# Performance work log

Measured on AMD Instinct MI355X. Metric: run time of the kernel, lower is better.

The kernel has to match this reference:

```python
import jax, jax.numpy as jnp
import numpy as np

N_NODES = 50000
N_EDGES = 800000
NODE_IN = 16
NODE_OUT = 3
H = 128
N_LAYERS = 3


def setup_inputs() -> dict:
    key = jax.random.key(0)
    ks = jax.random.split(key, 16)
    s = 0.05
    inp = {
        "x": jax.random.normal(ks[0], (N_NODES, NODE_IN), dtype=jnp.float32),
        "edge_index": jax.random.randint(ks[1], (2, N_EDGES), 0, N_NODES, dtype=jnp.int64),
        # encoder / decoder
        "enc_w": jax.random.normal(ks[2], (NODE_IN, H), dtype=jnp.float32) * s,
        "enc_b": jnp.zeros((H,), dtype=jnp.float32),
        "dec_w": jax.random.normal(ks[3], (H, NODE_OUT), dtype=jnp.float32) * s,
        "dec_b": jnp.zeros((NODE_OUT,), dtype=jnp.float32),
        # 3 processor layers, edge MLP: Linear(2H,H) -> ReLU -> Linear(H,H)
        "edge_w1": jax.random.normal(ks[4], (N_LAYERS, 2 * H, H), dtype=jnp.float32) * s,
        "edge_b1": jnp.zeros((N_LAYERS, H), dtype=jnp.float32),
        "edge_w2": jax.random.normal(ks[5], (N_LAYERS, H, H), dtype=jnp.float32) * s,
        "edge_b2": jnp.zeros((N_LAYERS, H), dtype=jnp.float32),
        # node MLP: Linear(2H,H) -> ReLU -> Linear(H,H)
        "node_w1": jax.random.normal(ks[6], (N_LAYERS, 2 * H, H), dtype=jnp.float32) * s,
        "node_b1": jnp.zeros((N_LAYERS, H), dtype=jnp.float32),
        "node_w2": jax.random.normal(ks[7], (N_LAYERS, H, H), dtype=jnp.float32) * s,
        "node_b2": jnp.zeros((N_LAYERS, H), dtype=jnp.float32),
    }
    return inp


def reference(x, edge_index, enc_w, enc_b, dec_w, dec_b,
              edge_w1, edge_b1, edge_w2, edge_b2,
              node_w1, node_b1, node_w2, node_b2):
    row = edge_index[0]  # source nodes
    col = edge_index[1]  # destination nodes
    h = x @ enc_w + enc_b  # [N, H]
    for l in range(N_LAYERS):
        # EdgeModel: cat(src, dest) -> MLP
        e_in = jnp.concatenate([h[row], h[col]], axis=1)  # [E, 2H]
        e = jnp.maximum(e_in @ edge_w1[l] + edge_b1[l], 0.0) @ edge_w2[l] + edge_b2[l]  # [E, H]
        # NodeModel: scatter_add messages by col, cat with x -> MLP
        agg = jax.ops.segment_sum(e, col, num_segments=h.shape[0])  # [N, H]
        n_in = jnp.concatenate([h, agg], axis=1)  # [N, 2H]
        h_upd = jnp.maximum(n_in @ node_w1[l] + node_b1[l], 0.0) @ node_w2[l] + node_b2[l]
        h = h + h_upd  # residual
    return h @ dec_w + dec_b  # [N, NODE_OUT]
```

## Files before the change

### kernel.cpp

```cpp
#include <hip/hip_runtime.h>
#include <hip/hip_bf16.h>
#include <stdint.h>

#define N_NODES 50000
#define N_EDGES 800000
#define HID 128
#define NODE_IN 16
#define NODE_OUT 3
#define NODE_TILES 782
#define SCAN_BLOCKS 196
#define EDGE_BLOCKS 3125
#define MFOLD_BLOCKS 192
#define DGB 16
#define EDBLOCKS 3125

typedef __attribute__((ext_vector_type(8))) short short8;
typedef __attribute__((ext_vector_type(4))) float f32x4;
typedef __attribute__((ext_vector_type(4))) unsigned int u32x4;

__device__ __forceinline__ unsigned short f2bf(float f) {
    union { float f; unsigned int u; } v; v.f = f;
    unsigned int u = v.u;
    u += 0x7fff + ((u >> 16) & 1);
    return (unsigned short)(u >> 16);
}
__device__ __forceinline__ float bf2f(unsigned short s) {
    union { unsigned int u; float f; } v; v.u = ((unsigned int)s) << 16;
    return v.f;
}
__device__ __forceinline__ float bfu_lo(unsigned int u) {
    union { unsigned int u; float f; } v; v.u = u << 16; return v.f;
}
__device__ __forceinline__ float bfu_hi(unsigned int u) {
    union { unsigned int u; float f; } v; v.u = u & 0xffff0000u; return v.f;
}
__device__ __forceinline__ unsigned int cvt_pk_bf16(float lo, float hi) {
    unsigned int r;
    asm("v_cvt_pk_bf16_f32 %0, %1, %2" : "=v"(r) : "v"(lo), "v"(hi));
    return r;
}

__global__ __launch_bounds__(256) void k1_fused(
    const int* __restrict__ colp, int* __restrict__ cnt, int* __restrict__ rank,
    const float* __restrict__ edge_w2, const float* __restrict__ node_w1,
    const float* __restrict__ edge_b2,
    float* __restrict__ Mtmp, float* __restrict__ Vtmp,
    const float* __restrict__ x, const float* __restrict__ enc_w,
    const float* __restrict__ enc_b, unsigned short* __restrict__ h) {
    __shared__ float wts[NODE_IN * HID];
    __shared__ float bts[HID];
    __shared__ float xs[64][NODE_IN];
    int b = blockIdx.x, t = threadIdx.x;
    if (b < EDGE_BLOCKS) {
        int e = b * 256 + t;
        rank[e] = atomicAdd(&cnt[colp[e]], 1);
    } else if (b < EDGE_BLOCKS + MFOLD_BLOCKS) {
        int d = (b - EDGE_BLOCKS) * 256 + t;
        int L = d / 16384, rem = d & 16383;
        int k = rem >> 7, n = rem & 127;
        const float* w2  = edge_w2 + (size_t)L * 16384;
        const float* w1b = node_w1 + (size_t)L * 32768 + 16384;
        float acc = 0.f;
        #pragma unroll 4
        for (int j = 0; j < 128; j++) acc += w2[k * 128 + j] * w1b[j * 128 + n];
        Mtmp[d] = acc;
        if (k == 0) {
            const float* b2 = edge_b2 + (size_t)L * 128;
            float vv = 0.f;
            #pragma unroll 4
            for (int j = 0; j < 128; j++) vv += b2[j] * w1b[j * 128 + n];
            Vtmp[L * 128 + n] = vv;
        }
    } else {
        int b2 = b - EDGE_BLOCKS - MFOLD_BLOCKS;
        int n0 = b2 * 64;
        for (int i = t; i < NODE_IN * HID; i += 256) wts[i] = enc_w[i];
        if (t < HID) bts[t] = enc_b[t];
        for (int i = t; i < 64 * NODE_IN; i += 256) {
            int nl = i >> 4, ii = i & 15;
            int n = n0 + nl;
            xs[nl][ii] = (n < N_NODES) ? x[n * NODE_IN + ii] : 0.f;
        }
        __syncthreads();
        for (int o = t; o < 64 * HID; o += 256) {
            int nl = o >> 7, cc = o & 127;
            float acc = bts[cc];
            #pragma unroll
            for (int i = 0; i < NODE_IN; i++) acc += xs[nl][i] * wts[i * HID + cc];
            int n = n0 + nl;
            if (n < N_NODES) h[n * HID + cc] = f2bf(acc);
        }
    }
}

__global__ __launch_bounds__(256) void k2a_scan1_swizzle(
    const int* __restrict__ cnt, int* __restrict__ ex, int* __restrict__ bsums,
    const float* __restrict__ edge_w1, const float* __restrict__ node_w1,
    const float* __restrict__ node_w2, const float* __restrict__ Mtmp,
    unsigned short* __restrict__ swz) {
    __shared__ int s[256];
    int b = blockIdx.x, t = threadIdx.x;
    if (b < SCAN_BLOCKS) {
        int i = b * 256 + t;
        int v = (i < N_NODES) ? cnt[i] : 0;
        s[t] = v;
        __syncthreads();
        for (int off = 1; off < 256; off <<= 1) {
            int u = (t >= off) ? s[t - off] : 0;
            __syncthreads();
            s[t] += u;
            __syncthreads();
        }
        if (i < N_NODES) ex[i] = s[t] - v;
        if (t == 255) bsums[b] = s[255];
    } else {
        for (int d = (b - SCAN_BLOCKS) * 256 + t; d < 3 * 98304;
             d += (gridDim.x - SCAN_BLOCKS) * 256) {
            int L = d / 98304;
            int rem = d - L * 98304;
            unsigned short* base = swz + L * 98304;
            if (rem < 32768) {
                const float* w1 = edge_w1 + (size_t)L * 32768;
                int j = rem & 7, ll = (rem >> 3) & 63, tt = rem >> 9;
                int nt = tt & 15, kt = tt >> 4;
                int k = kt * 32 + ((ll >> 4) << 3) + j;
                int cc = nt * 16 + (ll & 15);
                float v = (cc < 128) ? w1[k * 128 + cc] : w1[(128 + k) * 128 + (cc - 128)];
                base[rem] = f2bf(v);
            } else if (rem < 49152) {
            } else if (rem < 81920) {
                int d2 = rem - 49152;
                int j = d2 & 7, ll = (d2 >> 3) & 63, tt = d2 >> 9;
                int nt = tt & 7, kt = tt >> 3;
                int k = kt * 32 + ((ll >> 4) << 3) + j, n = (nt << 4) + (ll & 15);
                float v = (k < 128) ? node_w1[(size_t)L * 32768 + k * 128 + n]
                                    : Mtmp[(size_t)L * 16384 + (k - 128) * 128 + n];
                base[rem] = f2bf(v);
            } else {
                int d2 = rem - 81920;
                const float* src = node_w2 + (size_t)L * 16384;
                int j = d2 & 7, ll = (d2 >> 3) & 63, tt = d2 >> 9;
                int nt = tt & 7, kt = tt >> 3;
                int k = kt * 32 + ((ll >> 4) << 3) + j, n = (nt << 4) + (ll & 15);
                base[rem] = f2bf(src[k * 128 + n]);
            }
        }
    }
}

__global__ __launch_bounds__(256) void k3_scatter_sd(
    const int* __restrict__ rowp, const int* __restrict__ colp,
    const int* __restrict__ ex, const int* __restrict__ bsums,
    const int* __restrict__ rank, int* __restrict__ rsrt, int* __restrict__ ex2,
    const unsigned short* __restrict__ h, const unsigned short* __restrict__ w1c,
    const float* __restrict__ eb1,
    unsigned short* __restrict__ S, unsigned short* __restrict__ D) {
    __shared__ int sc[256];
    __shared__ int ls[SCAN_BLOCKS];
    __shared__ unsigned short hs[64][136];
    int b = blockIdx.x, t = threadIdx.x;
    if (b < EDGE_BLOCKS) {
        int v = (t < SCAN_BLOCKS) ? bsums[t] : 0;
        sc[t] = v;
        __syncthreads();
        for (int off = 1; off < 256; off <<= 1) {
            int u = (t >= off) ? sc[t - off] : 0;
            __syncthreads();
            sc[t] += u;
            __syncthreads();
        }
        if (t < SCAN_BLOCKS) ls[t] = sc[t] - v;
        __syncthreads();

        if (b < SCAN_BLOCKS) {
            int i = b * 256 + t;
            if (i < N_NODES) ex2[i] = ex[i] + ls[b];
        }
        int e = b * 256 + t;
        int c = colp[e];
        int pos = ex[c] + ls[c >> 8] + rank[e];
        rsrt[pos] = rowp[e];
    } else {
        int b2 = b - EDGE_BLOCKS;
        int wave = t >> 6, l = t & 63, q = l >> 4, l16 = l & 15;
        int nt0s = wave * 4;
        int n0 = b2 * 64;
        for (int i = t; i < 64 * 16; i += 256) {
            int nl = i >> 4, li = i & 15;
            int n = n0 + nl;
            short8 v = (short8){0, 0, 0, 0, 0, 0, 0, 0};
            if (n < N_NODES) v = *(const short8*)(h + (size_t)n * HID + li * 8);
            *(short8*)&hs[nl][li * 8] = v;
        }
        short8 wr[4][4];
        #pragma unroll
        for (int kt = 0; kt < 4; kt++)
            #pragma unroll
            for (int i = 0; i < 4; i++)
                wr[kt][i] = *(const short8*)(w1c + ((kt * 16 + nt0s + i) * 64 + l) * 8);
        __syncthreads();

        f32x4 acc[4][4];
        #pragma unroll
        for (int g = 0; g < 4; g++)
            #pragma unroll
            for (int i = 0; i < 4; i++) acc[g][i] = (f32x4){0.f, 0.f, 0.f, 0.f};
        #pragma unroll
        for (int kt = 0; kt < 4; kt++) {
            #pragma unroll
            for (int g = 0; g < 4; g++) {
                short8 a = *(const short8*)&hs[g * 16 + l16][kt * 32 + q * 8];
                #pragma unroll
                for (int i = 0; i < 4; i++)
                    acc[g][i] = __builtin_amdgcn_mfma_f32_16x16x32_bf16(a, wr[kt][i], acc[g][i], 0, 0, 0);
            }
        }
        #pragma unroll
        for (int i = 0; i < 4; i++) {
            int cc = (nt0s + i) * 16 + l16;
            float badd = 0.f;
            if (cc >= 128) badd = eb1[cc - 128];
            #pragma unroll
            for (int g = 0; g < 4; g++)
                #pragma unroll
                for (int r = 0; r < 4; r++) {
                    int n = n0 + g * 16 + q * 4 + r;
                    if (n < N_NODES) {
                        unsigned short v = f2bf(acc[g][i][r] + badd);
                        if (cc < 128) S[n * HID + cc] = v;
                        else          D[n * HID + (cc - 128)] = v;
                    }
                }
        }
    }
}

__global__ __launch_bounds__(256, 8) void edge_kernel(
    const unsigned short* __restrict__ S, const unsigned short* __restrict__ D,
    const int* __restrict__ rsrt, const int* __restrict__ ex2,
    float* __restrict__ aggH)
{
    int t = threadIdx.x;
    int g16 = t >> 4, ch = t & 15;

    const int q = EDBLOCKS / 8, r = EDBLOCKS % 8;
    int xcd = blockIdx.x & 7, slot = blockIdx.x >> 3;
    int cntx = q + (xcd < r);
    if (slot >= cntx) return;
    int myb = xcd * q + (xcd < r ? xcd : r) + slot;

    int d = myb * DGB + g16;
    int e0 = ex2[d];
    int e1 = (d < N_NODES - 1) ? ex2[d + 1] : N_EDGES;

    short8 dv = *(const short8*)(D + (size_t)d * HID + ch * 8);
    float dr[8];
    #pragma unroll
    for (int p = 0; p < 4; p++) {
        unsigned int ud = ((const unsigned int*)&dv)[p];
        dr[2 * p]     = bfu_lo(ud);
        dr[2 * p + 1] = bfu_hi(ud);
    }

    float a[8];
    #pragma unroll
    for (int j = 0; j < 8; j++) a[j] = 0.f;

    auto ldS = [&](int e) -> short8 {
        int rn = rsrt[e];
        return *(const short8*)(S + (size_t)rn * HID + ch * 8);
    };
    auto accum = [&](const short8& sv) {
        #pragma unroll
        for (int p = 0; p < 4; p++) {
            unsigned int us = ((const unsigned int*)&sv)[p];
            float v0 = bfu_lo(us) + dr[2 * p];
            float v1 = bfu_hi(us) + dr[2 * p + 1];
            v0 = v0 > 0.f ? v0 : 0.f;
            v1 = v1 > 0.f ? v1 : 0.f;
            a[2 * p]     += v0;
            a[2 * p + 1] += v1;
        }
    };

    int e = e0;
    short8 s0 = (short8){0, 0, 0, 0, 0, 0, 0, 0};
    short8 s1 = s0;
    if (e < e1)     s0 = ldS(e);
    if (e + 1 < e1) s1 = ldS(e + 1);
    for (; e + 2 < e1; e += 2) {
        short8 n0v = ldS(e + 2);
        short8 n1v = (e + 3 < e1) ? ldS(e + 3) : (short8){0, 0, 0, 0, 0, 0, 0, 0};
        accum(s0);
        accum(s1);
        s0 = n0v;
        s1 = n1v;
    }
    if (e < e1)     accum(s0);
    if (e + 1 < e1) accum(s1);

    f32x4* dst = (f32x4*)(aggH + (size_t)d * HID + ch * 8);
    dst[0] = (f32x4){a[0], a[1], a[2], a[3]};
    dst[1] = (f32x4){a[4], a[5], a[6], a[7]};
}

template<int LAST>
__global__ __launch_bounds__(256, 4) void node_kernel(
    unsigned short* __restrict__ h, float* __restrict__ aggH, const int* __restrict__ cnt,
    const unsigned short* __restrict__ w1m_s, const float* __restrict__ b1,
    const float* __restrict__ vfold,
    const unsigned short* __restrict__ w2s, const float* __restrict__ b2,
    const unsigned short* __restrict__ w1c_next, const float* __restrict__ eb1n,
    unsigned short* __restrict__ S, unsigned short* __restrict__ D,
    const float* __restrict__ dec_w, const float* __restrict__ dec_b, float* __restrict__ out)
{
    __shared__ unsigned short in_h[64][136];
    __shared__ unsigned short in_a[64][136];
    __shared__ int cnt_s[64];
    __shared__ float dw[HID * NODE_OUT];
    __shared__ float db[NODE_OUT];
    int t = threadIdx.x, wave = t >> 6, l = t & 63, q = l >> 4, l16 = l & 15;
    int nt0 = wave * 2, nt0s = wave * 4;
    int n0 = blockIdx.x * 64;

    if (LAST) {
        for (int i = t; i < HID * NODE_OUT; i += 256) dw[i] = dec_w[i];
        if (t < NODE_OUT) db[t] = dec_b[t];
    }

    #pragma unroll
    for (int it = 0; it < 8; it++) {
        int g = it * 256 + t;
        int nl = g >> 5, sub = g & 31, half = sub >> 4, li = sub & 15;
        int n = n0 + nl;
        short8 v = (short8){0, 0, 0, 0, 0, 0, 0, 0};
        if (n < N_NODES) {
            if (half == 0) {
                v = *(const short8*)(h + n * HID + li * 8);
            } else {
                const float* ap = aggH + n * HID + li * 8;
                f32x4 a0 = *(const f32x4*)ap, a1 = *(const f32x4*)(ap + 4);
                unsigned int* vp = (unsigned int*)&v;
                vp[0] = cvt_pk_bf16(a0[0], a0[1]);
                vp[1] = cvt_pk_bf16(a0[2], a0[3]);
                vp[2] = cvt_pk_bf16(a1[0], a1[1]);
                vp[3] = cvt_pk_bf16(a1[2], a1[3]);
            }
        }
        if (half == 0) *(short8*)&in_h[nl][li * 8] = v;
        else           *(short8*)&in_a[nl][li * 8] = v;
    }
    if (t < 64) cnt_s[t] = (n0 + t < N_NODES) ? cnt[n0 + t] : 0;
    __syncthreads();

    float b1r0 = b1[nt0 * 16 + l16], b1r1 = b1[(nt0 + 1) * 16 + l16];
    float vr0 = vfold[nt0 * 16 + l16], vr1 = vfold[(nt0 + 1) * 16 + l16];
    float b2r0 = b2[nt0 * 16 + l16], b2r1 = b2[(nt0 + 1) * 16 + l16];

    f32x4 acc[4][2];
    #pragma unroll
    for (int g = 0; g < 4; g++)
        #pragma unroll
        for (int j = 0; j < 2; j++) acc[g][j] = (f32x4){0.f, 0.f, 0.f, 0.f};
    #pragma unroll
    for (int kt = 0; kt < 8; kt++) {
        short8 b0 = *(const short8*)(w1m_s + ((kt * 8 + nt0)     * 64 + l) * 8);
        short8 b1v = *(const short8*)(w1m_s + ((kt * 8 + nt0 + 1) * 64 + l) * 8);
        #pragma unroll
        for (int g = 0; g < 4; g++) {
            short8 a = (kt < 4) ? *(const short8*)&in_h[g * 16 + l16][kt * 32 + q * 8]
                                : *(const short8*)&in_a[g * 16 + l16][(kt - 4) * 32 + q * 8];
            acc[g][0] = __builtin_amdgcn_mfma_f32_16x16x32_bf16(a, b0, acc[g][0], 0, 0, 0);
            acc[g][1] = __builtin_amdgcn_mfma_f32_16x16x32_bf16(a, b1v, acc[g][1], 0, 0, 0);
        }
    }
    __syncthreads();

    #pragma unroll
    for (int j = 0; j < 2; j++) {
        float bv = j ? b1r1 : b1r0;
        float vv = j ? vr1 : vr0;
        #pragma unroll
        for (int g = 0; g < 4; g++)
            #pragma unroll
            for (int r = 0; r < 4; r++) {
                int m2 = g * 16 + q * 4 + r;
                float v = acc[g][j][r] + bv + (float)cnt_s[m2] * vv;
                v = v > 0.f ? v : 0.f;
                in_a[m2][(nt0 + j) * 16 + l16] = f2bf(v);
            }
    }
    __syncthreads();

    f32x4 acc2[4][2];
    #pragma unroll
    for (int g = 0; g < 4; g++)
        #pragma unroll
        for (int j = 0; j < 2; j++) acc2[g][j] = (f32x4){0.f, 0.f, 0.f, 0.f};
    #pragma unroll
    for (int kt = 0; kt < 4; kt++) {
        short8 b0 = *(const short8*)(w2s + ((kt * 8 + nt0)     * 64 + l) * 8);
        short8 b1v = *(const short8*)(w2s + ((kt * 8 + nt0 + 1) * 64 + l) * 8);
        #pragma unroll
        for (int g = 0; g < 4; g++) {
            short8 a = *(const short8*)&in_a[g * 16 + l16][kt * 32 + q * 8];
            acc2[g][0] = __builtin_amdgcn_mfma_f32_16x16x32_bf16(a, b0, acc2[g][0], 0, 0, 0);
            acc2[g][1] = __builtin_amdgcn_mfma_f32_16x16x32_bf16(a, b1v, acc2[g][1], 0, 0, 0);
        }
    }
    #pragma unroll
    for (int j = 0; j < 2; j++) {
        float bv = j ? b2r1 : b2r0;
        #pragma unroll
        for (int g = 0; g < 4; g++)
            #pragma unroll
            for (int r = 0; r < 4; r++) {
                float v = acc2[g][j][r] + bv;
                int m2 = g * 16 + q * 4 + r;
                int n = n0 + m2;
                if (n < N_NODES) {
                    int c = (nt0 + j) * 16 + l16;
                    unsigned short nh = f2bf(bf2f(in_h[m2][c]) + v);
                    if (!LAST) h[n * HID + c] = nh;
                    in_h[m2][c] = nh;
                }
            }
    }
    __syncthreads();

    if (!LAST) {
        #pragma unroll
        for (int p = 0; p < 2; p++) {
            short8 wr[4][2];
            #pragma unroll
            for (int kt = 0; kt < 4; kt++) {
                wr[kt][0] = *(const short8*)(w1c_next + ((kt * 16 + nt0s + p * 2)     * 64 + l) * 8);
                wr[kt][1] = *(const short8*)(w1c_next + ((kt * 16 + nt0s + p * 2 + 1) * 64 + l) * 8);
            }
            f32x4 accs[4][2];
            #pragma unroll
            for (int g = 0; g < 4; g++)
                #pragma unroll
                for (int i = 0; i < 2; i++) accs[g][i] = (f32x4){0.f, 0.f, 0.f, 0.f};
            #pragma unroll
            for (int kt = 0; kt < 4; kt++) {
                #pragma unroll
                for (int g = 0; g < 4; g++) {
                    short8 a = *(const short8*)&in_h[g * 16 + l16][kt * 32 + q * 8];
                    accs[g][0] = __builtin_amdgcn_mfma_f32_16x16x32_bf16(a, wr[kt][0], accs[g][0], 0, 0, 0);
                    accs[g][1] = __builtin_amdgcn_mfma_f32_16x16x32_bf16(a, wr[kt][1], accs[g][1], 0, 0, 0);
                }
            }
            #pragma unroll
            for (int i = 0; i < 2; i++) {
                int c = (nt0s + p * 2 + i) * 16 + l16;
                float badd = 0.f;
                if (c >= 128) badd = eb1n[c - 128];
                #pragma unroll
                for (int g = 0; g < 4; g++)
                    #pragma unroll
                    for (int r = 0; r < 4; r++) {
                        int n = n0 + g * 16 + q * 4 + r;
                        if (n < N_NODES) {
                            unsigned short v = f2bf(accs[g][i][r] + badd);
                            if (c < 128) S[n * HID + c] = v;
                            else         D[n * HID + (c - 128)] = v;
                        }
                    }
            }
        }
    } else {
        if (t < 64 * NODE_OUT) {
            int nl = t / 3, o = t - 3 * nl;
            int n = n0 + nl;
            if (n < N_NODES) {
                float a = db[o];
                #pragma unroll 4
                for (int k = 0; k < HID; k++) a += bf2f(in_h[nl][k]) * dw[k * 3 + o];
                out[n * 3 + o] = a;
            }
        }
    }
}

extern "C" void kernel_launch(void* const* d_in, const int* in_sizes, int n_in,
                              void* d_out, int out_size, void* d_ws, size_t ws_size,
                              hipStream_t stream) {
    const float* x       = (const float*)d_in[0];
    const int*   ei      = (const int*)d_in[1];
    const float* enc_w   = (const float*)d_in[2];
    const float* enc_b   = (const float*)d_in[3];
    const float* dec_w   = (const float*)d_in[4];
    const float* dec_b   = (const float*)d_in[5];
    const float* edge_w1 = (const float*)d_in[6];
    const float* edge_b1 = (const float*)d_in[7];
    const float* edge_w2 = (const float*)d_in[8];
    const float* edge_b2 = (const float*)d_in[9];
    const float* node_w1 = (const float*)d_in[10];
    const float* node_b1 = (const float*)d_in[11];
    const float* node_w2 = (const float*)d_in[12];
    const float* node_b2 = (const float*)d_in[13];

    char* ws = (char*)d_ws;
    unsigned short* h    = (unsigned short*)ws;
    float*          aggH = (float*)(ws + 12800000);
    unsigned short* swz  = (unsigned short*)(ws + 38400000);
    int* cnt             = (int*)(ws + 38989824);
    int* ex              = (int*)(ws + 39189824);
    int* bsums           = (int*)(ws + 39389824);
    int* rsrt            = (int*)(ws + 39390848);
    unsigned short* Sbuf = (unsigned short*)(ws + 45790848);
    unsigned short* Dbuf = (unsigned short*)(ws + 58590848);
    float* Mtmp          = (float*)(ws + 71390848);
    float* Vtmp          = (float*)(ws + 71587456);
    int* ex2             = (int*)(ws + 71588992);
    int* rank            = (int*)(ws + 72000000);

    const int* rowp = ei;
    const int* colp = ei + N_EDGES;

    hipMemsetAsync(cnt, 0, (size_t)N_NODES * 4, stream);

    k1_fused<<<EDGE_BLOCKS + MFOLD_BLOCKS + NODE_TILES, 256, 0, stream>>>(
        colp, cnt, rank, edge_w2, node_w1, edge_b2, Mtmp, Vtmp,
        x, enc_w, enc_b, h);
    k2a_scan1_swizzle<<<SCAN_BLOCKS + 288, 256, 0, stream>>>(cnt, ex, bsums, edge_w1,
                                                             node_w1, node_w2, Mtmp, swz);
    k3_scatter_sd<<<EDGE_BLOCKS + NODE_TILES, 256, 0, stream>>>(
        rowp, colp, ex, bsums, rank, rsrt, ex2,
        h, swz , edge_b1 , Sbuf, Dbuf);

    for (int L = 0; L < 3; L++) {
        unsigned short* base = swz + (size_t)L * 98304;
        unsigned short* next = swz + (size_t)(L + 1) * 98304;
        edge_kernel<<<3128, 256, 0, stream>>>(Sbuf, Dbuf, rsrt, ex2, aggH);
        if (L < 2) {
            node_kernel<0><<<NODE_TILES, 256, 0, stream>>>(
                h, aggH, cnt,
                base + 49152, node_b1 + (size_t)L * HID, Vtmp + (size_t)L * HID,
                base + 81920, node_b2 + (size_t)L * HID,
                next, edge_b1 + (size_t)(L + 1) * HID, Sbuf, Dbuf, dec_w, dec_b, (float*)d_out);
        } else {
            node_kernel<1><<<NODE_TILES, 256, 0, stream>>>(
                h, aggH, cnt,
                base + 49152, node_b1 + (size_t)L * HID, Vtmp + (size_t)L * HID,
                base + 81920, node_b2 + (size_t)L * HID,
                base , edge_b1 , Sbuf, Dbuf, dec_w, dec_b, (float*)d_out);
        }
    }
}
```

Measured before the change: 364.9 us.

## Store aggregates as bf16, deepen edge gather prefetch, split weight swizzle across kernels

The edge kernel now writes per-node aggregated messages as packed bf16 instead of fp32, halving the aggregate buffer traffic, and the node kernel reads them directly without converting. The edge gather loop is restructured with an 8-deep prefetch of source indices and 4-deep prefetch of S rows to hide gather latency. The edge_w1 and node_w2 swizzles move into the first fused kernel, leaving only the Mtmp-dependent node_w1 swizzle in the scan kernel. The bf16 aggregate adds rounding before the node MLP, and the extra prefetch raises register pressure.

Result: slower. 415.1 us (+13.7%).

```diff
diff --git a/kernel.cpp b/kernel.cpp
--- a/kernel.cpp
+++ b/kernel.cpp
@@ -11,6 +11,8 @@
 #define SCAN_BLOCKS 196
 #define EDGE_BLOCKS 3125
 #define MFOLD_BLOCKS 192
+#define SWZA_BLOCKS 576
+#define SWZB_BLOCKS 384
 #define DGB 16
 #define EDBLOCKS 3125
 
@@ -46,7 +48,9 @@
     const float* __restrict__ edge_b2,
     float* __restrict__ Mtmp, float* __restrict__ Vtmp,
     const float* __restrict__ x, const float* __restrict__ enc_w,
-    const float* __restrict__ enc_b, unsigned short* __restrict__ h) {
+    const float* __restrict__ enc_b, unsigned short* __restrict__ h,
+    const float* __restrict__ edge_w1, const float* __restrict__ node_w2,
+    unsigned short* __restrict__ swz) {
     __shared__ float wts[NODE_IN * HID];
     __shared__ float bts[HID];
     __shared__ float xs[64][NODE_IN];
@@ -71,7 +75,7 @@
             for (int j = 0; j < 128; j++) vv += b2[j] * w1b[j * 128 + n];
             Vtmp[L * 128 + n] = vv;
         }
-    } else {
+    } else if (b < EDGE_BLOCKS + MFOLD_BLOCKS + NODE_TILES) {
         int b2 = b - EDGE_BLOCKS - MFOLD_BLOCKS;
         int n0 = b2 * 64;
         for (int i = t; i < NODE_IN * HID; i += 256) wts[i] = enc_w[i];
@@ -90,13 +94,32 @@
             int n = n0 + nl;
             if (n < N_NODES) h[n * HID + cc] = f2bf(acc);
         }
+    } else {
+        int d = (b - EDGE_BLOCKS - MFOLD_BLOCKS - NODE_TILES) * 256 + t;
+        int L = d / 49152, rem2 = d - L * 49152;
+        unsigned short* base = swz + L * 98304;
+        if (rem2 < 32768) {
+            const float* w1 = edge_w1 + (size_t)L * 32768;
+            int j = rem2 & 7, ll = (rem2 >> 3) & 63, tt = rem2 >> 9;
+            int nt = tt & 15, kt = tt >> 4;
+            int k = kt * 32 + ((ll >> 4) << 3) + j;
+            int cc = nt * 16 + (ll & 15);
+            float v = (cc < 128) ? w1[k * 128 + cc] : w1[(128 + k) * 128 + (cc - 128)];
+            base[rem2] = f2bf(v);
+        } else {
+            int d2 = rem2 - 32768;
+            const float* src = node_w2 + (size_t)L * 16384;
+            int j = d2 & 7, ll = (d2 >> 3) & 63, tt = d2 >> 9;
+            int nt = tt & 7, kt = tt >> 3;
+            int k = kt * 32 + ((ll >> 4) << 3) + j, n = (nt << 4) + (ll & 15);
+            base[81920 + d2] = f2bf(src[k * 128 + n]);
+        }
     }
 }
 
 __global__ __launch_bounds__(256) void k2a_scan1_swizzle(
     const int* __restrict__ cnt, int* __restrict__ ex, int* __restrict__ bsums,
-    const float* __restrict__ edge_w1, const float* __restrict__ node_w1,
-    const float* __restrict__ node_w2, const float* __restrict__ Mtmp,
+    const float* __restrict__ node_w1, const float* __restrict__ Mtmp,
     unsigned short* __restrict__ swz) {
     __shared__ int s[256];
     int b = blockIdx.x, t = threadIdx.x;
@@ -114,37 +137,15 @@
         if (i < N_NODES) ex[i] = s[t] - v;
         if (t == 255) bsums[b] = s[255];
     } else {
-        for (int d = (b - SCAN_BLOCKS) * 256 + t; d < 3 * 98304;
-             d += (gridDim.x - SCAN_BLOCKS) * 256) {
-            int L = d / 98304;
-            int rem = d - L * 98304;
-            unsigned short* base = swz + L * 98304;
-            if (rem < 32768) {
-                const float* w1 = edge_w1 + (size_t)L * 32768;
-                int j = rem & 7, ll = (rem >> 3) & 63, tt = rem >> 9;
-                int nt = tt & 15, kt = tt >> 4;
-                int k = kt * 32 + ((ll >> 4) << 3) + j;
-                int cc = nt * 16 + (ll & 15);
-                float v = (cc < 128) ? w1[k * 128 + cc] : w1[(128 + k) * 128 + (cc - 128)];
-                base[rem] = f2bf(v);
-            } else if (rem < 49152) {
-            } else if (rem < 81920) {
-                int d2 = rem - 49152;
-                int j = d2 & 7, ll = (d2 >> 3) & 63, tt = d2 >> 9;
-                int nt = tt & 7, kt = tt >> 3;
-                int k = kt * 32 + ((ll >> 4) << 3) + j, n = (nt << 4) + (ll & 15);
-                float v = (k < 128) ? node_w1[(size_t)L * 32768 + k * 128 + n]
-                                    : Mtmp[(size_t)L * 16384 + (k - 128) * 128 + n];
-                base[rem] = f2bf(v);
-            } else {
-                int d2 = rem - 81920;
-                const float* src = node_w2 + (size_t)L * 16384;
-                int j = d2 & 7, ll = (d2 >> 3) & 63, tt = d2 >> 9;
-                int nt = tt & 7, kt = tt >> 3;
-                int k = kt * 32 + ((ll >> 4) << 3) + j, n = (nt << 4) + (ll & 15);
-                base[rem] = f2bf(src[k * 128 + n]);
-            }
-        }
+        int d = (b - SCAN_BLOCKS) * 256 + t;
+        int L = d / 32768, d2 = d - L * 32768;
+        unsigned short* base = swz + L * 98304;
+        int j = d2 & 7, ll = (d2 >> 3) & 63, tt = d2 >> 9;
+        int nt = tt & 7, kt = tt >> 3;
+        int k = kt * 32 + ((ll >> 4) << 3) + j, n = (nt << 4) + (ll & 15);
+        float v = (k < 128) ? node_w1[(size_t)L * 32768 + k * 128 + n]
+                            : Mtmp[(size_t)L * 16384 + (k - 128) * 128 + n];
+        base[49152 + d2] = f2bf(v);
     }
 }
 
@@ -238,7 +239,7 @@
 __global__ __launch_bounds__(256, 8) void edge_kernel(
     const unsigned short* __restrict__ S, const unsigned short* __restrict__ D,
     const int* __restrict__ rsrt, const int* __restrict__ ex2,
-    float* __restrict__ aggH)
+    unsigned short* __restrict__ aggB)
 {
     int t = threadIdx.x;
     int g16 = t >> 4, ch = t & 15;
@@ -254,6 +255,25 @@
     int e1 = (d < N_NODES - 1) ? ex2[d + 1] : N_EDGES;
 
     short8 dv = *(const short8*)(D + (size_t)d * HID + ch * 8);
+
+    auto Srow = [&](int rn) -> short8 {
+        return *(const short8*)(S + (size_t)rn * HID + ch * 8);
+    };
+    const short8 z = (short8){0, 0, 0, 0, 0, 0, 0, 0};
+
+    int ra0 = (e0     < e1) ? rsrt[e0]     : 0;
+    int ra1 = (e0 + 1 < e1) ? rsrt[e0 + 1] : 0;
+    int ra2 = (e0 + 2 < e1) ? rsrt[e0 + 2] : 0;
+    int ra3 = (e0 + 3 < e1) ? rsrt[e0 + 3] : 0;
+    int rb0 = (e0 + 4 < e1) ? rsrt[e0 + 4] : 0;
+    int rb1 = (e0 + 5 < e1) ? rsrt[e0 + 5] : 0;
+    int rb2 = (e0 + 6 < e1) ? rsrt[e0 + 6] : 0;
+    int rb3 = (e0 + 7 < e1) ? rsrt[e0 + 7] : 0;
+    short8 c0 = (e0     < e1) ? Srow(ra0) : z;
+    short8 c1 = (e0 + 1 < e1) ? Srow(ra1) : z;
+    short8 c2 = (e0 + 2 < e1) ? Srow(ra2) : z;
+    short8 c3 = (e0 + 3 < e1) ? Srow(ra3) : z;
+
     float dr[8];
     #pragma unroll
     for (int p = 0; p < 4; p++) {
@@ -261,52 +281,54 @@
         dr[2 * p]     = bfu_lo(ud);
         dr[2 * p + 1] = bfu_hi(ud);
     }
-
     float a[8];
     #pragma unroll
     for (int j = 0; j < 8; j++) a[j] = 0.f;
 
-    auto ldS = [&](int e) -> short8 {
-        int rn = rsrt[e];
-        return *(const short8*)(S + (size_t)rn * HID + ch * 8);
-    };
     auto accum = [&](const short8& sv) {
         #pragma unroll
         for (int p = 0; p < 4; p++) {
             unsigned int us = ((const unsigned int*)&sv)[p];
             float v0 = bfu_lo(us) + dr[2 * p];
             float v1 = bfu_hi(us) + dr[2 * p + 1];
-            v0 = v0 > 0.f ? v0 : 0.f;
-            v1 = v1 > 0.f ? v1 : 0.f;
-            a[2 * p]     += v0;
-            a[2 * p + 1] += v1;
+            a[2 * p]     += v0 > 0.f ? v0 : 0.f;
+            a[2 * p + 1] += v1 > 0.f ? v1 : 0.f;
         }
     };
 
     int e = e0;
-    short8 s0 = (short8){0, 0, 0, 0, 0, 0, 0, 0};
-    short8 s1 = s0;
-    if (e < e1)     s0 = ldS(e);
-    if (e + 1 < e1) s1 = ldS(e + 1);
-    for (; e + 2 < e1; e += 2) {
-        short8 n0v = ldS(e + 2);
-        short8 n1v = (e + 3 < e1) ? ldS(e + 3) : (short8){0, 0, 0, 0, 0, 0, 0, 0};
-        accum(s0);
-        accum(s1);
-        s0 = n0v;
-        s1 = n1v;
-    }
-    if (e < e1)     accum(s0);
-    if (e + 1 < e1) accum(s1);
-
-    f32x4* dst = (f32x4*)(aggH + (size_t)d * HID + ch * 8);
-    dst[0] = (f32x4){a[0], a[1], a[2], a[3]};
-    dst[1] = (f32x4){a[4], a[5], a[6], a[7]};
+    while (e + 12 <= e1) {
+        int m0 = rsrt[e + 8], m1 = rsrt[e + 9];
+        short8 f0 = Srow(rb0), f1 = Srow(rb1);
+        accum(c0); accum(c1);
+        int m2 = rsrt[e + 10], m3 = rsrt[e + 11];
+        short8 f2 = Srow(rb2), f3 = Srow(rb3);
+        accum(c2); accum(c3);
+        c0 = f0; c1 = f1; c2 = f2; c3 = f3;
+        rb0 = m0; rb1 = m1; rb2 = m2; rb3 = m3;
+        e += 4;
+    }
+    int rem = e1 - e;
+    if (rem > 0) accum(c0);
+    if (rem > 1) accum(c1);
+    if (rem > 2) accum(c2);
+    if (rem > 3) accum(c3);
+    if (rem > 4) accum(Srow(rb0));
+    if (rem > 5) accum(Srow(rb1));
+    if (rem > 6) accum(Srow(rb2));
+    if (rem > 7) accum(Srow(rb3));
+    for (int j = 8; j < rem; j++) accum(Srow(rsrt[e + j]));
+
+    u32x4 oa;
+    #pragma unroll
+    for (int p = 0; p < 4; p++) oa[p] = cvt_pk_bf16(a[2 * p], a[2 * p + 1]);
+    *(u32x4*)(aggB + (size_t)d * HID + ch * 8) = oa;
 }
 
 template<int LAST>
 __global__ __launch_bounds__(256, 4) void node_kernel(
-    unsigned short* __restrict__ h, float* __restrict__ aggH, const int* __restrict__ cnt,
+    unsigned short* __restrict__ h, const unsigned short* __restrict__ aggB,
+    const int* __restrict__ cnt,
     const unsigned short* __restrict__ w1m_s, const float* __restrict__ b1,
     const float* __restrict__ vfold,
     const unsigned short* __restrict__ w2s, const float* __restrict__ b2,
@@ -335,17 +357,8 @@
         int n = n0 + nl;
         short8 v = (short8){0, 0, 0, 0, 0, 0, 0, 0};
         if (n < N_NODES) {
-            if (half == 0) {
-                v = *(const short8*)(h + n * HID + li * 8);
-            } else {
-                const float* ap = aggH + n * HID + li * 8;
-                f32x4 a0 = *(const f32x4*)ap, a1 = *(const f32x4*)(ap + 4);
-                unsigned int* vp = (unsigned int*)&v;
-                vp[0] = cvt_pk_bf16(a0[0], a0[1]);
-                vp[1] = cvt_pk_bf16(a0[2], a0[3]);
-                vp[2] = cvt_pk_bf16(a1[0], a1[1]);
-                vp[3] = cvt_pk_bf16(a1[2], a1[3]);
-            }
+            if (half == 0) v = *(const short8*)(h + (size_t)n * HID + li * 8);
+            else           v = *(const short8*)(aggB + (size_t)n * HID + li * 8);
         }
         if (half == 0) *(short8*)&in_h[nl][li * 8] = v;
         else           *(short8*)&in_a[nl][li * 8] = v;
@@ -503,29 +516,29 @@
 
     char* ws = (char*)d_ws;
     unsigned short* h    = (unsigned short*)ws;
-    float*          aggH = (float*)(ws + 12800000);
-    unsigned short* swz  = (unsigned short*)(ws + 38400000);
-    int* cnt             = (int*)(ws + 38989824);
-    int* ex              = (int*)(ws + 39189824);
-    int* bsums           = (int*)(ws + 39389824);
-    int* rsrt            = (int*)(ws + 39390848);
-    unsigned short* Sbuf = (unsigned short*)(ws + 45790848);
-    unsigned short* Dbuf = (unsigned short*)(ws + 58590848);
-    float* Mtmp          = (float*)(ws + 71390848);
-    float* Vtmp          = (float*)(ws + 71587456);
-    int* ex2             = (int*)(ws + 71588992);
-    int* rank            = (int*)(ws + 72000000);
+    unsigned short* aggB = (unsigned short*)(ws + 12800000);
+    unsigned short* swz  = (unsigned short*)(ws + 25600000);
+    int* cnt             = (int*)(ws + 26189824);
+    int* ex              = (int*)(ws + 26389824);
+    int* bsums           = (int*)(ws + 26589824);
+    int* rsrt            = (int*)(ws + 26590848);
+    unsigned short* Sbuf = (unsigned short*)(ws + 29790848);
+    unsigned short* Dbuf = (unsigned short*)(ws + 42590848);
+    float* Mtmp          = (float*)(ws + 55390848);
+    float* Vtmp          = (float*)(ws + 55587456);
+    int* ex2             = (int*)(ws + 55588992);
+    int* rank            = (int*)(ws + 55788992);
 
     const int* rowp = ei;
     const int* colp = ei + N_EDGES;
 
     hipMemsetAsync(cnt, 0, (size_t)N_NODES * 4, stream);
 
-    k1_fused<<<EDGE_BLOCKS + MFOLD_BLOCKS + NODE_TILES, 256, 0, stream>>>(
+    k1_fused<<<EDGE_BLOCKS + MFOLD_BLOCKS + NODE_TILES + SWZA_BLOCKS, 256, 0, stream>>>(
         colp, cnt, rank, edge_w2, node_w1, edge_b2, Mtmp, Vtmp,
-        x, enc_w, enc_b, h);
-    k2a_scan1_swizzle<<<SCAN_BLOCKS + 288, 256, 0, stream>>>(cnt, ex, bsums, edge_w1,
-                                                             node_w1, node_w2, Mtmp, swz);
+        x, enc_w, enc_b, h, edge_w1, node_w2, swz);
+    k2a_scan1_swizzle<<<SCAN_BLOCKS + SWZB_BLOCKS, 256, 0, stream>>>(
+        cnt, ex, bsums, node_w1, Mtmp, swz);
     k3_scatter_sd<<<EDGE_BLOCKS + NODE_TILES, 256, 0, stream>>>(
         rowp, colp, ex, bsums, rank, rsrt, ex2,
         h, swz , edge_b1 , Sbuf, Dbuf);
@@ -533,16 +546,16 @@
     for (int L = 0; L < 3; L++) {
         unsigned short* base = swz + (size_t)L * 98304;
         unsigned short* next = swz + (size_t)(L + 1) * 98304;
-        edge_kernel<<<3128, 256, 0, stream>>>(Sbuf, Dbuf, rsrt, ex2, aggH);
+        edge_kernel<<<3128, 256, 0, stream>>>(Sbuf, Dbuf, rsrt, ex2, aggB);
         if (L < 2) {
             node_kernel<0><<<NODE_TILES, 256, 0, stream>>>(
-                h, aggH, cnt,
+                h, aggB, cnt,
                 base + 49152, node_b1 + (size_t)L * HID, Vtmp + (size_t)L * HID,
                 base + 81920, node_b2 + (size_t)L * HID,
                 next, edge_b1 + (size_t)(L + 1) * HID, Sbuf, Dbuf, dec_w, dec_b, (float*)d_out);
         } else {
             node_kernel<1><<<NODE_TILES, 256, 0, stream>>>(
-                h, aggH, cnt,
+                h, aggB, cnt,
                 base + 49152, node_b1 + (size_t)L * HID, Vtmp + (size_t)L * HID,
                 base + 81920, node_b2 + (size_t)L * HID,
                 base , edge_b1 , Sbuf, Dbuf, dec_w, dec_b, (float*)d_out);
```
